# Optimization experiments

Measured on AMD Instinct MI355X. Metric: run time of the kernel, lower is better.

## Reference

```python
import jax, jax.numpy as jnp
import numpy as np

HEADS = 12
LN_EPS = 1e-12
NUM_PROTOTYPES = 8


def _layer_norm(x, g, b):
    mu = x.mean(-1, keepdims=True)
    var = ((x - mu) ** 2).mean(-1, keepdims=True)
    return (x - mu) / jnp.sqrt(var + LN_EPS) * g + b


def _bert_attention(q_in, kv_in, wq, bq, wk, bk, wv, bv, wo, bo, ln_g, ln_b):
    # HF BertAttention: MHA (query from q_in, key/value from kv_in) then
    # SelfOutput: dense + residual(q_in) + LayerNorm. Dropout = 0 (eval).
    B, Sq, D = q_in.shape
    Sk = kv_in.shape[1]
    dh = D // HEADS
    q = (q_in @ wq + bq).reshape(B, Sq, HEADS, dh).transpose(0, 2, 1, 3)
    k = (kv_in @ wk + bk).reshape(B, Sk, HEADS, dh).transpose(0, 2, 1, 3)
    v = (kv_in @ wv + bv).reshape(B, Sk, HEADS, dh).transpose(0, 2, 1, 3)
    scores = jnp.einsum('bhqd,bhkd->bhqk', q, k) / jnp.sqrt(jnp.asarray(dh, q.dtype))
    probs = jax.nn.softmax(scores, axis=-1)
    ctx = jnp.einsum('bhqk,bhkd->bhqd', probs, v).transpose(0, 2, 1, 3).reshape(B, Sq, D)
    return _layer_norm(ctx @ wo + bo + q_in, ln_g, ln_b)


def setup_inputs() -> dict:
    key = jax.random.key(0)
    ks = jax.random.split(key, 16)
    D = 768
    inp = {
        'local_feats': jax.random.normal(ks[0], (8, 256, D), jnp.float32),
        'global_feat_dict': jax.random.normal(ks[1], (16384, D), jnp.float32),
    }
    i = 2
    for pre in ('ll', 'lg'):
        for nm in ('wq', 'wk', 'wv', 'wo'):
            inp[f'{pre}_{nm}'] = 0.02 * jax.random.normal(ks[i], (D, D), jnp.float32)
            i += 1
        for nm in ('bq', 'bk', 'bv', 'bo'):
            inp[f'{pre}_{nm}'] = jnp.zeros((D,), jnp.float32)
        inp[f'{pre}_ln_g'] = jnp.ones((D,), jnp.float32)
        inp[f'{pre}_ln_b'] = jnp.zeros((D,), jnp.float32)
    inp['ln_g'] = jnp.ones((D,), jnp.float32)
    inp['ln_b'] = jnp.zeros((D,), jnp.float32)
    inp['aug_w'] = 0.02 * jax.random.normal(ks[i], (D, 1), jnp.float32)
    inp['ori_w'] = 0.02 * jax.random.normal(ks[i + 1], (D, 1), jnp.float32)
    inp['aug_b'] = jnp.zeros((1,), jnp.float32)
    inp['ori_b'] = jnp.zeros((1,), jnp.float32)
    return inp


def reference(local_feats, global_feat_dict,
              ll_wq, ll_bq, ll_wk, ll_bk, ll_wv, ll_bv, ll_wo, ll_bo, ll_ln_g, ll_ln_b,
              lg_wq, lg_bq, lg_wk, lg_bk, lg_wv, lg_bv, lg_wo, lg_bo, lg_ln_g, lg_ln_b,
              ln_g, ln_b, aug_w, aug_b, ori_w, ori_b):
    B, L, D = local_feats.shape
    K = NUM_PROTOTYPES
    # similarity_topk retrieval: cosine similarity against prototype pool
    g_norm = global_feat_dict / jnp.linalg.norm(global_feat_dict, axis=-1, keepdims=True)
    t_norm = local_feats / jnp.linalg.norm(local_feats, axis=-1, keepdims=True)
    sim = jnp.einsum('bld,nd->bln', t_norm, g_norm)          # [B, L, N]
    topk_idx = jax.lax.top_k(sim, K)[1]                       # [B, L, K]
    global_feats = global_feat_dict[topk_idx].reshape(B, L * K, D)
    # self-attn over locals, cross-attn locals -> retrieved prototypes
    ll = _bert_attention(local_feats, local_feats,
                         ll_wq, ll_bq, ll_wk, ll_bk, ll_wv, ll_bv, ll_wo, ll_bo, ll_ln_g, ll_ln_b)
    lg = _bert_attention(local_feats, global_feats,
                         lg_wq, lg_bq, lg_wk, lg_bk, lg_wv, lg_bv, lg_wo, lg_bo, lg_ln_g, lg_ln_b)
    out = _layer_norm(ll + lg, ln_g, ln_b)
    aug_weight = jax.nn.sigmoid(out @ aug_w + aug_b + local_feats @ ori_w + ori_b)
    return aug_weight * out + (1.0 - aug_weight) * local_feats
```

## Files before the change

### kernel.cpp

```cpp
#include <hip/hip_runtime.h>
#include <math.h>

#define D     768
#define HEADS 12
#define DH    64
#define BATCH 8
#define LSEQ  256
#define MROWS 2048
#define NDICT 16384
#define TOPK  8

typedef _Float16 half_t;
typedef half_t half8 __attribute__((ext_vector_type(8)));
typedef float floatx4 __attribute__((ext_vector_type(4)));

#define F_DICT 0u
#define F_DKV  6291456u
#define F_TN   18874368u
#define F_LOC  19660800u
#define F_WT   20447232u
#define F_BF   22806528u
#define F_TOPI 22814720u
#define F_LP   22831104u
#define F_CTX  25976832u
#define F_D1   26763264u
#define F_D3   28336128u
#define F_ML   31481856u
#define F_CANDV 31678464u
#define F_CANDI 31809536u
#define F_NRM  31940608u
#define F_USED 31956992u
#define F_ROWMAP 31973376u
#define F_INVMAP 31989760u
#define F_CNT  32006144u

typedef const __attribute__((address_space(1))) void* gptr_as1;
typedef __attribute__((address_space(3))) void* lptr_as3;
#define GLDS16(gp, lp) __builtin_amdgcn_global_load_lds((gptr_as1)(gp), (lptr_as3)(lp), 16, 0, 0)

__device__ __forceinline__ float bsum(float v, float* red) {
  int t = threadIdx.x;
#pragma unroll
  for (int d = 32; d > 0; d >>= 1) v += __shfl_xor(v, d);
  if ((t & 63) == 0) red[t >> 6] = v;
  __syncthreads();
  float r = red[0] + red[1] + red[2] + red[3];
  __syncthreads();
  return r;
}

__global__ __launch_bounds__(256) void k_prep_wt(
    const float* __restrict__ dict, const float* __restrict__ local,
    half_t* __restrict__ gdict_h, float* __restrict__ dnrm,
    half_t* __restrict__ loc_h, half_t* __restrict__ tn_h,
    const float* w0, const float* w1, const float* w2, const float* w3,
    const float* w4, const float* w5, const float* w6, const float* w7,
    const float* b0, const float* b1, const float* b2, const float* b3,
    const float* b4, const float* b5, const float* b6, const float* b7,
    half_t* __restrict__ Wt, float* __restrict__ bfout) {
  __shared__ float red[8];
  __shared__ float tile[32][33];
  int g = blockIdx.x, t = threadIdx.x;
  if (g < NDICT) {
    const float* xr = dict + (size_t)g * D;
    float v0 = xr[t], v1 = xr[t + 256], v2 = xr[t + 512];
    float s = bsum(v0*v0 + v1*v1 + v2*v2, red);
    float n = sqrtf(s), inv = 1.0f / n;
    half_t* yr = gdict_h + (size_t)g * D;
    yr[t] = (half_t)(v0*inv); yr[t+256] = (half_t)(v1*inv); yr[t+512] = (half_t)(v2*inv);
    if (t == 0) dnrm[g] = n;
  } else if (g < NDICT + MROWS) {
    size_t r = g - NDICT;
    const float* xr = local + r * (size_t)D;
    float v0 = xr[t], v1 = xr[t + 256], v2 = xr[t + 512];
    float s = bsum(v0*v0 + v1*v1 + v2*v2, red);
    float inv = 1.0f / sqrtf(s);
    half_t* rr = loc_h + r * (size_t)D;
    half_t* nr = tn_h + r * (size_t)D;
    rr[t] = (half_t)v0;        rr[t+256] = (half_t)v1;        rr[t+512] = (half_t)v2;
    nr[t] = (half_t)(v0*inv);  nr[t+256] = (half_t)(v1*inv);  nr[t+512] = (half_t)(v2*inv);
  } else {
    const float* wsrcs[8] = {w0,w1,w2,w3,w4,w5,w6,w7};
    const float* bsrcs[8] = {b0,b1,b2,b3,b4,b5,b6,b7};
    int id = g - (NDICT + MROWS);
    int z = id / 576, rem = id % 576;
    int by = rem / 24, bx = rem % 24;
    const float* Wsrc = wsrcs[z];
    half_t* dst = Wt + (size_t)z * D * D;
    int tx = t & 31, ty = t >> 5;
    int c0 = bx * 32, r0 = by * 32;
#pragma unroll
    for (int j = 0; j < 4; j++)
      tile[ty + j*8][tx] = Wsrc[(size_t)(r0 + ty + j*8) * D + c0 + tx];
    __syncthreads();
#pragma unroll
    for (int j = 0; j < 4; j++)
      dst[(size_t)(c0 + ty + j*8) * D + r0 + tx] = (half_t)tile[tx][ty + j*8];
    if (bx == 0 && by == 0) {
#pragma unroll
      for (int j = 0; j < 3; j++)
        bfout[z * D + t + j*256] = bsrcs[z][t + j*256];
    }
  }
}

__device__ __forceinline__ void hgemm_core(
    const half_t* __restrict__ A, const half_t* __restrict__ B,
    const float* __restrict__ bias, const float* __restrict__ dnrm,
    const int* __restrict__ rowmap, void* __restrict__ Cout,
    int N, int K, int outHalf, int bx, int by, int mhalf,
    half_t* As, half_t* Bs) {
  int tid = threadIdx.x;
  int wid = tid >> 6, lane = tid & 63;
  int l16 = lane & 15, quad = lane >> 4;
  int n0 = bx * 128, m0 = by * 128;
  if (mhalf && m0 >= mhalf) { B += (size_t)D * D; if (bias) bias += D; }
  int wm = (wid & 1) * 64, wn = (wid >> 1) * 64;

  int r0  = tid >> 3;
  int cbg = (tid & 7) ^ (r0 & 7);
  const half_t* Aps[4];
#pragma unroll
  for (int i = 0; i < 4; i++) {
    int mm = m0 + r0 + 32*i;
    int mr = rowmap ? rowmap[mm] : mm;
    Aps[i] = A + (size_t)mr * K + cbg * 8;
  }
  const half_t* Bp = B + (size_t)(n0 + r0) * K + cbg * 8;

  floatx4 acc[4][4];
#pragma unroll
  for (int i = 0; i < 4; i++)
#pragma unroll
    for (int j = 0; j < 4; j++) { acc[i][j][0]=0.f; acc[i][j][1]=0.f; acc[i][j][2]=0.f; acc[i][j][3]=0.f; }

  for (int k0 = 0; k0 < K; k0 += 64) {
#pragma unroll
    for (int i = 0; i < 4; i++)
      GLDS16(Aps[i] + k0, As + ((size_t)i*256 + wid*64) * 8);
#pragma unroll
    for (int i = 0; i < 4; i++)
      GLDS16(Bp + k0 + (size_t)i * 32 * K, Bs + ((size_t)i*256 + wid*64) * 8);
    __syncthreads();
#pragma unroll
    for (int ks = 0; ks < 2; ks++) {
      half8 af[4], bf[4];
#pragma unroll
      for (int i = 0; i < 4; i++) {
        int row = wm + i*16 + l16;
        int cb = (quad + ks*4) ^ (row & 7);
        af[i] = *(const half8*)&As[row*64 + cb*8];
      }
#pragma unroll
      for (int j = 0; j < 4; j++) {
        int row = wn + j*16 + l16;
        int cb = (quad + ks*4) ^ (row & 7);
        bf[j] = *(const half8*)&Bs[row*64 + cb*8];
      }
#pragma unroll
      for (int i = 0; i < 4; i++)
#pragma unroll
        for (int j = 0; j < 4; j++)
          acc[i][j] = __builtin_amdgcn_mfma_f32_16x16x32_f16(af[i], bf[j], acc[i][j], 0, 0, 0);
    }
    __syncthreads();
  }

  float bcol[4];
#pragma unroll
  for (int j = 0; j < 4; j++) bcol[j] = bias ? bias[n0 + wn + j*16 + l16] : 0.f;
  if (outHalf) {
    half_t* C = (half_t*)Cout;
#pragma unroll
    for (int i = 0; i < 4; i++)
#pragma unroll
      for (int r = 0; r < 4; r++) {
        int grow = m0 + wm + i*16 + quad*4 + r;
        float sc = dnrm ? dnrm[rowmap ? rowmap[grow] : grow] : 1.0f;
#pragma unroll
        for (int j = 0; j < 4; j++)
          C[(size_t)grow * N + n0 + wn + j*16 + l16] = (half_t)(acc[i][j][r] * sc + bcol[j]);
      }
  } else {
    float* C = (float*)Cout;
#pragma unroll
    for (int i = 0; i < 4; i++)
#pragma unroll
      for (int r = 0; r < 4; r++) {
        int grow = m0 + wm + i*16 + quad*4 + r;
        float sc = dnrm ? dnrm[rowmap ? rowmap[grow] : grow] : 1.0f;
#pragma unroll
        for (int j = 0; j < 4; j++)
          C[(size_t)grow * N + n0 + wn + j*16 + l16] = acc[i][j][r] * sc + bcol[j];
      }
  }
}

__global__ __launch_bounds__(256) void k_gemm_simlp(
    const half_t* __restrict__ tn, const half_t* __restrict__ gd,
    half_t* __restrict__ sim,
    const half_t* __restrict__ loc, const half_t* __restrict__ wt0,
    const float* __restrict__ bf0, half_t* __restrict__ lp) {
  __shared__ half_t As[128*64];
  __shared__ half_t Bs[128*64];
  int gid = blockIdx.x;
  if (gid < 2048) {
    int bx = (gid & 7) + ((gid >> 3) / 16) * 8;
    int by = (gid >> 3) % 16;
    hgemm_core(tn, gd, nullptr, nullptr, nullptr, sim, NDICT, D, 1, bx, by, 0, As, Bs);
  } else {
    int rel = gid - 2048;
    int bx = (rel & 7) + ((rel >> 3) / 16) * 8;
    int by = (rel >> 3) % 16;
    hgemm_core(loc, wt0, bf0, nullptr, nullptr, lp, 3072, D, 1, bx, by, 0, As, Bs);
  }
}

__global__ __launch_bounds__(256) void k_gemm_dkv(
    const half_t* __restrict__ gd, const half_t* __restrict__ wt4,
    const float* __restrict__ bf4, const float* __restrict__ dnrm,
    const int* __restrict__ rowmap, const int* __restrict__ cnt,
    half_t* __restrict__ dkv) {
  __shared__ half_t As[128*64];
  __shared__ half_t Bs[128*64];
  int mceil = (*cnt + 127) & ~127;
  if ((int)blockIdx.y * 128 >= mceil) return;
  hgemm_core(gd, wt4, bf4, dnrm, rowmap, dkv, 1536, D, 1, blockIdx.x, blockIdx.y, 0, As, Bs);
}

__global__ __launch_bounds__(256) void k_gemm_wo(
    const half_t* __restrict__ ctx, const half_t* __restrict__ wt6,
    const float* __restrict__ bf6, float* __restrict__ dd) {
  __shared__ half_t As[128*64];
  __shared__ half_t Bs[128*64];
  hgemm_core(ctx, wt6, bf6, nullptr, nullptr, dd, D, D, 0, blockIdx.x, blockIdx.y, MROWS, As, Bs);
}

__global__ __launch_bounds__(256) void k_topk1(const half_t* __restrict__ sim,
                                               float* __restrict__ candv,
                                               int* __restrict__ candi,
                                               int* __restrict__ used,
                                               int* __restrict__ rowmap,
                                               int* __restrict__ cnt) {
  int t = threadIdx.x;
  if (t < 4) used[blockIdx.x * 4 + t] = 0;
  else if (t < 8) rowmap[blockIdx.x * 4 + t - 4] = 0;
  if (blockIdx.x == 0 && t == 8) *cnt = 0;

  int gw = blockIdx.x * 4 + (t >> 6);
  int lane = t & 63;
  int row = gw >> 3, seg = gw & 7;
  int cbase = seg * 2048;
  const half_t* p = sim + (size_t)row * NDICT + cbase;

  float v[32];
#pragma unroll
  for (int i = 0; i < 4; i++) {
    half8 h = *(const half8*)(p + i*512 + lane*8);
#pragma unroll
    for (int j = 0; j < 8; j++) v[i*8 + j] = (float)h[j];
  }
  float m = v[0]; int pos = 0;
#pragma unroll
  for (int i = 1; i < 32; i++) { if (v[i] > m) { m = v[i]; pos = i; } }

  for (int it = 0; it < 8; it++) {
    int gidx = cbase + (pos >> 3) * 512 + lane * 8 + (pos & 7);
    float bv = m; int bi = gidx;
#pragma unroll
    for (int d2 = 1; d2 < 64; d2 <<= 1) {
      float ov = __shfl_xor(bv, d2); int oi = __shfl_xor(bi, d2);
      if (ov > bv || (ov == bv && oi < bi)) { bv = ov; bi = oi; }
    }
    if (lane == 0) {
      size_t base = (size_t)row * 64 + seg * 8 + it;
      candv[base] = bv; candi[base] = bi;
    }
    if (bi == gidx) {
      v[pos] = -INFINITY;
      m = v[0]; pos = 0;
#pragma unroll
      for (int i = 1; i < 32; i++) { if (v[i] > m) { m = v[i]; pos = i; } }
    }
  }
}

__global__ __launch_bounds__(256) void k_topk2(const float* __restrict__ candv,
                                               const int* __restrict__ candi,
                                               int* __restrict__ topi,
                                               int* __restrict__ used) {
  int row = blockIdx.x * 4 + (threadIdx.x >> 6);
  int lane = threadIdx.x & 63;
  float v = candv[(size_t)row * 64 + lane];
  int id = candi[(size_t)row * 64 + lane];
#pragma unroll
  for (int it = 0; it < 8; it++) {
    float bv = v; int bi = id;
#pragma unroll
    for (int d2 = 1; d2 < 64; d2 <<= 1) {
      float ov = __shfl_xor(bv, d2); int oi = __shfl_xor(bi, d2);
      if (ov > bv || (ov == bv && oi < bi)) { bv = ov; bi = oi; }
    }
    if (lane == 0) { topi[row * 8 + it] = bi; used[bi] = 1; }
    if (id == bi) { v = -INFINITY; id = 0x7FFFFFFF; }
  }
}

__global__ __launch_bounds__(256) void k_cmp(const int* __restrict__ used,
                                             int* __restrict__ rowmap,
                                             int* __restrict__ invmap,
                                             int* __restrict__ cnt) {
  int i = blockIdx.x * 256 + threadIdx.x;
  if (used[i]) { int s = atomicAdd(cnt, 1); rowmap[s] = i; invmap[i] = s; }
}
__global__ __launch_bounds__(256) void k_remap(int* __restrict__ topi,
                                               const int* __restrict__ invmap) {
  int i = blockIdx.x * 256 + threadIdx.x;
  topi[i] = invmap[topi[i]];
}

__global__ __launch_bounds__(256) void k_flash2(
    const half_t* __restrict__ lp, const half_t* __restrict__ dkv,
    const int* __restrict__ topi_,
    half_t* __restrict__ ctx_ll, half_t* __restrict__ Opart, float* __restrict__ ml) {
  __shared__ half_t Ks[64][72];
  __shared__ half_t Vt[64][72];
  __shared__ half_t Ps[4][16][72];

  int tid = threadIdx.x;
  int wid = tid >> 6;
  int lane = tid & 63;
  int l16 = lane & 15, quad = lane >> 4;

  const half_t *Q, *K, *V; const int* kidx; half_t* Out;
  int qS, kvS, Sk, ns, rel;
  if (blockIdx.x < BATCH*HEADS*4*4) {
    rel = blockIdx.x;
    Q = lp + 2304; qS = 3072; K = dkv; V = dkv + 768; kvS = 1536;
    kidx = topi_; Sk = LSEQ*TOPK; ns = 4; Out = nullptr;
  } else {
    rel = blockIdx.x - BATCH*HEADS*4*4;
    Q = lp; qS = 3072; K = lp + 768; V = lp + 1536; kvS = 3072;
    kidx = nullptr; Sk = LSEQ; ns = 1; Out = ctx_ll;
  }

  int sp = rel % ns;
  int rest = rel / ns;
  int qt = rest & 3;
  int h  = (rest >> 2) % HEADS;
  int bb = rest / (4 * HEADS);
  int q0 = qt * 64 + wid * 16;
  int sLen = Sk / ns, s0 = sp * sLen;

  const float SCL = 0.125f * 1.4426950408889634f;
  const half_t* qrow = Q + (size_t)(bb * LSEQ + q0 + l16) * qS + h * DH;
  half8 aq0 = *(const half8*)(qrow + quad*8);
  half8 aq1 = *(const half8*)(qrow + 32 + quad*8);

  floatx4 o[4];
#pragma unroll
  for (int nt = 0; nt < 4; nt++) { o[nt][0]=0.f; o[nt][1]=0.f; o[nt][2]=0.f; o[nt][3]=0.f; }
  float mreg[4] = {-INFINITY, -INFINITY, -INFINITY, -INFINITY};
  float lreg[4] = {0.f, 0.f, 0.f, 0.f};

  for (int k0 = s0; k0 < s0 + sLen; k0 += 64) {
    {
      int row = tid >> 2, cg = tid & 3;
      int key = k0 + row;
      size_t rowid = kidx ? (size_t)kidx[(size_t)bb * Sk + key]
                          : (size_t)(bb * LSEQ + key);
      const half_t* kb = K + rowid * (size_t)kvS + h * DH + cg * 16;
      const half_t* vb = V + rowid * (size_t)kvS + h * DH + cg * 16;
      *(half8*)&Ks[row][cg*16]     = *(const half8*)kb;
      *(half8*)&Ks[row][cg*16 + 8] = *(const half8*)(kb + 8);
      half8 v0 = *(const half8*)vb, v1 = *(const half8*)(vb + 8);
#pragma unroll
      for (int jj = 0; jj < 8; jj++) { Vt[cg*16 + jj][row] = v0[jj]; Vt[cg*16 + 8 + jj][row] = v1[jj]; }
    }
    __syncthreads();

    floatx4 c[4];
#pragma unroll
    for (int nt = 0; nt < 4; nt++) {
      half8 b0 = *(const half8*)&Ks[nt*16 + l16][quad*8];
      half8 b1 = *(const half8*)&Ks[nt*16 + l16][32 + quad*8];
      floatx4 z; z[0]=0.f; z[1]=0.f; z[2]=0.f; z[3]=0.f;
      z = __builtin_amdgcn_mfma_f32_16x16x32_f16(aq0, b0, z, 0, 0, 0);
      z = __builtin_amdgcn_mfma_f32_16x16x32_f16(aq1, b1, z, 0, 0, 0);
      c[nt] = z;
    }

    float alpha[4];
#pragma unroll
    for (int r = 0; r < 4; r++) {
      float mx = fmaxf(fmaxf(c[0][r], c[1][r]), fmaxf(c[2][r], c[3][r]));
      mx = fmaxf(mx, __shfl_xor(mx, 1));
      mx = fmaxf(mx, __shfl_xor(mx, 2));
      mx = fmaxf(mx, __shfl_xor(mx, 4));
      mx = fmaxf(mx, __shfl_xor(mx, 8));
      float mn = fmaxf(mreg[r], mx);
      float al = __builtin_amdgcn_exp2f((mreg[r] - mn) * SCL);
      float ps = 0.f;
#pragma unroll
      for (int nt = 0; nt < 4; nt++) {
        float p = __builtin_amdgcn_exp2f((c[nt][r] - mn) * SCL);
        c[nt][r] = p; ps += p;
      }
      ps += __shfl_xor(ps, 1);
      ps += __shfl_xor(ps, 2);
      ps += __shfl_xor(ps, 4);
      ps += __shfl_xor(ps, 8);
      mreg[r] = mn; lreg[r] = lreg[r] * al + ps; alpha[r] = al;
    }

#pragma unroll
    for (int nt = 0; nt < 4; nt++)
#pragma unroll
      for (int r = 0; r < 4; r++)
        Ps[wid][quad*4 + r][nt*16 + l16] = (half_t)c[nt][r];
    half8 p0 = *(const half8*)&Ps[wid][l16][quad*8];
    half8 p1 = *(const half8*)&Ps[wid][l16][32 + quad*8];

#pragma unroll
    for (int nt = 0; nt < 4; nt++)
#pragma unroll
      for (int r = 0; r < 4; r++) o[nt][r] *= alpha[r];
#pragma unroll
    for (int nt = 0; nt < 4; nt++) {
      half8 v0 = *(const half8*)&Vt[nt*16 + l16][quad*8];
      half8 v1 = *(const half8*)&Vt[nt*16 + l16][32 + quad*8];
      o[nt] = __builtin_amdgcn_mfma_f32_16x16x32_f16(p0, v0, o[nt], 0, 0, 0);
      o[nt] = __builtin_amdgcn_mfma_f32_16x16x32_f16(p1, v1, o[nt], 0, 0, 0);
    }
    __syncthreads();
  }

  if (ns == 1) {
    half_t* ob = Out + (size_t)(bb * LSEQ + q0 + quad*4) * D + h * DH;
#pragma unroll
    for (int r = 0; r < 4; r++) {
      float inv = 1.0f / lreg[r];
#pragma unroll
      for (int nt = 0; nt < 4; nt++)
        ob[(size_t)r * D + nt*16 + l16] = (half_t)(o[nt][r] * inv);
    }
  } else {
    size_t rbase = (size_t)sp * MROWS + bb * LSEQ + q0 + quad*4;
    half_t* ob = Opart + rbase * D + h * DH;
#pragma unroll
    for (int r = 0; r < 4; r++) {
      float inv = 1.0f / lreg[r];
#pragma unroll
      for (int nt = 0; nt < 4; nt++)
        ob[(size_t)r * D + nt*16 + l16] = (half_t)(o[nt][r] * inv);
    }
    if (l16 == 0) {
#pragma unroll
      for (int r = 0; r < 4; r++) {
        size_t mi = ((rbase + r) * HEADS + h) * 2;
        ml[mi] = mreg[r]; ml[mi + 1] = lreg[r];
      }
    }
  }
}

__global__ __launch_bounds__(256) void k_comb(const half_t* __restrict__ Op,
                                              const float* __restrict__ ml,
                                              half_t* __restrict__ ctx) {
  int r = blockIdx.x, t = threadIdx.x;
  const float SCL = 0.125f * 1.4426950408889634f;
#pragma unroll
  for (int i = 0; i < 3; i++) {
    int col = t + i*256;
    int h = col >> 6;
    float m[4], l[4];
    float ms = -INFINITY;
#pragma unroll
    for (int s = 0; s < 4; s++) {
      size_t mi = (((size_t)s * MROWS + r) * HEADS + h) * 2;
      m[s] = ml[mi]; l[s] = ml[mi + 1];
      ms = fmaxf(ms, m[s]);
    }
    float den = 0.f, num = 0.f;
#pragma unroll
    for (int s = 0; s < 4; s++) {
      float w = __builtin_amdgcn_exp2f((m[s] - ms) * SCL) * l[s];
      den += w;
      num += w * (float)Op[((size_t)s * MROWS + r) * D + col];
    }
    ctx[(size_t)r * D + col] = (half_t)(num / den);
  }
}

__global__ __launch_bounds__(256) void k_lngate3(
    const float* __restrict__ dd, const float* __restrict__ loc,
    const float* __restrict__ llg, const float* __restrict__ llb,
    const float* __restrict__ lgg, const float* __restrict__ lgb,
    const float* __restrict__ lng, const float* __restrict__ lnb,
    const float* __restrict__ aw, const float* __restrict__ ow,
    const float* __restrict__ ab, const float* __restrict__ orb,
    float* __restrict__ y) {
  __shared__ float red[8];
  size_t r = blockIdx.x; int t = threadIdx.x;
  const float* ar = dd + r*(size_t)D;
  const float* br = dd + ((size_t)MROWS + r)*(size_t)D;
  const float* lcl = loc + r*(size_t)D;
  float l0 = lcl[t], l1 = lcl[t+256], l2 = lcl[t+512];

  float a0 = ar[t]+l0, a1 = ar[t+256]+l1, a2 = ar[t+512]+l2;
  float mu = bsum(a0+a1+a2, red) * (1.0f/768.0f);
  float d0 = a0-mu, d1 = a1-mu, d2 = a2-mu;
  float var = bsum(d0*d0 + d1*d1 + d2*d2, red) * (1.0f/768.0f);
  float rstd = rsqrtf(var + 1e-12f);
  float x0 = d0*rstd*llg[t]     + llb[t];
  float x1 = d1*rstd*llg[t+256] + llb[t+256];
  float x2 = d2*rstd*llg[t+512] + llb[t+512];

  float b0 = br[t]+l0, b1 = br[t+256]+l1, b2 = br[t+512]+l2;
  mu = bsum(b0+b1+b2, red) * (1.0f/768.0f);
  d0 = b0-mu; d1 = b1-mu; d2 = b2-mu;
  var = bsum(d0*d0 + d1*d1 + d2*d2, red) * (1.0f/768.0f);
  rstd = rsqrtf(var + 1e-12f);
  x0 += d0*rstd*lgg[t]     + lgb[t];
  x1 += d1*rstd*lgg[t+256] + lgb[t+256];
  x2 += d2*rstd*lgg[t+512] + lgb[t+512];

  mu = bsum(x0+x1+x2, red) * (1.0f/768.0f);
  d0 = x0-mu; d1 = x1-mu; d2 = x2-mu;
  var = bsum(d0*d0 + d1*d1 + d2*d2, red) * (1.0f/768.0f);
  rstd = rsqrtf(var + 1e-12f);
  float o0 = d0*rstd*lng[t]     + lnb[t];
  float o1 = d1*rstd*lng[t+256] + lnb[t+256];
  float o2 = d2*rstd*lng[t+512] + lnb[t+512];

  float s = o0*aw[t] + l0*ow[t]
          + o1*aw[t+256] + l1*ow[t+256]
          + o2*aw[t+512] + l2*ow[t+512];
  float z = bsum(s, red) + ab[0] + orb[0];
  float w = 1.0f / (1.0f + __expf(-z));
  float* yr = y + r*(size_t)D;
  yr[t]     = w*o0 + (1.f-w)*l0;
  yr[t+256] = w*o1 + (1.f-w)*l1;
  yr[t+512] = w*o2 + (1.f-w)*l2;
}

extern "C" void kernel_launch(void* const* d_in, const int* in_sizes, int n_in,
                              void* d_out, int out_size, void* d_ws, size_t ws_size,
                              hipStream_t stream) {
  (void)in_sizes; (void)n_in; (void)out_size; (void)ws_size;
  const float* local = (const float*)d_in[0];
  const float* dict  = (const float*)d_in[1];
  const float* ll_g  = (const float*)d_in[10];
  const float* ll_b  = (const float*)d_in[11];
  const float* lg_g  = (const float*)d_in[20];
  const float* lg_b  = (const float*)d_in[21];
  const float* ln_g  = (const float*)d_in[22];
  const float* ln_b  = (const float*)d_in[23];
  const float* aug_w = (const float*)d_in[24];
  const float* ori_w = (const float*)d_in[25];
  const float* aug_b = (const float*)d_in[26];
  const float* ori_b = (const float*)d_in[27];

  float* W = (float*)d_ws;
  half_t* gdict_h = (half_t*)(W + F_DICT);
  half_t* sim_h   = (half_t*)(W + F_DKV);
  half_t* dkv     = (half_t*)(W + F_DKV);
  half_t* tn_h    = (half_t*)(W + F_TN);
  half_t* loc_h   = (half_t*)(W + F_LOC);
  half_t* wt      = (half_t*)(W + F_WT);
  float*  bf      = W + F_BF;
  int*    topi    = (int*)(W + F_TOPI);
  half_t* lp      = (half_t*)(W + F_LP);
  half_t* ctx_ll  = (half_t*)(W + F_CTX);
  half_t* ctx_lg  = (half_t*)(W + F_D1);
  half_t* Opart   = (half_t*)(W + F_D1);
  float*  dd      = W + F_D3;
  float*  ml      = W + F_ML;
  float*  candv   = W + F_CANDV;
  int*    candi   = (int*)(W + F_CANDI);
  float*  dnrm    = W + F_NRM;
  int*    used    = (int*)(W + F_USED);
  int*    rowmap  = (int*)(W + F_ROWMAP);
  int*    invmap  = (int*)(W + F_INVMAP);
  int*    cnt     = (int*)(W + F_CNT);

  dim3 blk(256);
  const size_t WS = (size_t)D * D;

  k_prep_wt<<<NDICT + MROWS + 4608, blk, 0, stream>>>(
      dict, local, gdict_h, dnrm, loc_h, tn_h,
      (const float*)d_in[2], (const float*)d_in[3], (const float*)d_in[4],
      (const float*)d_in[12], (const float*)d_in[13], (const float*)d_in[14],
      (const float*)d_in[5], (const float*)d_in[15],
      (const float*)d_in[6], (const float*)d_in[7], (const float*)d_in[8],
      (const float*)d_in[16], (const float*)d_in[17], (const float*)d_in[18],
      (const float*)d_in[9], (const float*)d_in[19], wt, bf);

  k_gemm_simlp<<<2048 + 384, blk, 0, stream>>>(tn_h, gdict_h, sim_h,
                                               loc_h, wt + 0*WS, bf + 0, lp);

  k_topk1<<<MROWS*8/4, blk, 0, stream>>>(sim_h, candv, candi, used, rowmap, cnt);
  k_topk2<<<MROWS/4, blk, 0, stream>>>(candv, candi, topi, used);
  k_cmp<<<64, blk, 0, stream>>>(used, rowmap, invmap, cnt);
  k_remap<<<64, blk, 0, stream>>>(topi, invmap);

  k_gemm_dkv<<<dim3(12, 128), blk, 0, stream>>>(
      gdict_h, wt + 4*WS, bf + 3072, dnrm, rowmap, cnt, dkv);

  k_flash2<<<dim3(BATCH*HEADS*4*4 + BATCH*HEADS*4), blk, 0, stream>>>(
      lp, dkv, topi, ctx_ll, Opart, ml);
  k_comb<<<MROWS, blk, 0, stream>>>(Opart, ml, ctx_lg);

  k_gemm_wo<<<dim3(6, 32), blk, 0, stream>>>(ctx_ll, wt + 6*WS, bf + 4608, dd);

  k_lngate3<<<MROWS, blk, 0, stream>>>(dd, local,
      ll_g, ll_b, lg_g, lg_b, ln_g, ln_b,
      aug_w, ori_w, aug_b, ori_b, (float*)d_out);
}
```

Before: 434.6 us.

## Use 256x256 double-buffered 512-thread GEMM tiles for similarity and KV projections

Adds a new GEMM core that computes 256x256 output tiles with 512 threads and double-buffered LDS staging via direct global-to-LDS loads, so the next K-slice loads while MFMAs run. The similarity/local-projection GEMM and the dictionary KV GEMM now use it, with a new XCD-aware block swizzle and fewer, larger blocks. The workspace is relaid out so the sim, dkv and dd buffers alias. Larger tiles cut global traffic per FLOP but use much more LDS and registers per block, which lowers occupancy. The candidate-skip granularity in the dkv GEMM also becomes coarser (256 rows).

```diff
diff --git a/kernel.cpp b/kernel.cpp
--- a/kernel.cpp
+++ b/kernel.cpp
@@ -14,25 +14,24 @@
 typedef half_t half8 __attribute__((ext_vector_type(8)));
 typedef float floatx4 __attribute__((ext_vector_type(4)));
 
-#define F_DICT 0u
-#define F_DKV  6291456u
-#define F_TN   18874368u
-#define F_LOC  19660800u
-#define F_WT   20447232u
-#define F_BF   22806528u
-#define F_TOPI 22814720u
-#define F_LP   22831104u
-#define F_CTX  25976832u
-#define F_D1   26763264u
-#define F_D3   28336128u
-#define F_ML   31481856u
-#define F_CANDV 31678464u
-#define F_CANDI 31809536u
-#define F_NRM  31940608u
-#define F_USED 31956992u
-#define F_ROWMAP 31973376u
-#define F_INVMAP 31989760u
-#define F_CNT  32006144u
+#define F_DICT   0u
+#define F_TN     6291456u
+#define F_LOC    7077888u
+#define F_WT     7864320u
+#define F_BF     10223616u
+#define F_TOPI   10231808u
+#define F_LP     10248192u
+#define F_SIM    13393920u
+#define F_CTX    30171136u
+#define F_D1     30957568u
+#define F_CANDV  30957568u
+#define F_CANDI  31088640u
+#define F_ML     34103296u
+#define F_NRM    34299904u
+#define F_USED   34316288u
+#define F_ROWMAP 34332672u
+#define F_INVMAP 34349056u
+#define F_CNT    34365440u
 
 typedef const __attribute__((address_space(1))) void* gptr_as1;
 typedef __attribute__((address_space(3))) void* lptr_as3;
@@ -196,36 +195,146 @@
   }
 }
 
-__global__ __launch_bounds__(256) void k_gemm_simlp(
+__device__ __forceinline__ void hgemm256_core(
+    const half_t* __restrict__ A, const half_t* __restrict__ B,
+    const float* __restrict__ bias, const float* __restrict__ dnrm,
+    const int* __restrict__ rowmap, half_t* __restrict__ C,
+    int N, int K, int bx, int by,
+    half_t* As0, half_t* As1, half_t* Bs0, half_t* Bs1) {
+  const int tid = threadIdx.x;
+  const int wid = tid >> 6, lane = tid & 63;
+  const int l16 = lane & 15, quad = lane >> 4;
+  const int m0 = by * 256, n0 = bx * 256;
+
+  const int r0 = tid >> 3;
+  const int cg = (tid & 7) ^ (r0 & 7);
+  const half_t* Aps[4]; const half_t* Bps[4];
+#pragma unroll
+  for (int i = 0; i < 4; i++) {
+    int mm = m0 + r0 + i * 64;
+    int mr = rowmap ? rowmap[mm] : mm;
+    Aps[i] = A + (size_t)mr * K + cg * 8;
+    Bps[i] = B + (size_t)(n0 + r0 + i * 64) * K + cg * 8;
+  }
+
+  const int arow = (wid & 3) * 32 + l16;
+  const int brow = (wid >> 2) * 64 + l16;
+  const int cb0 = (quad ^ (l16 & 7)) * 8;
+  const int cb1 = ((quad + 4) ^ (l16 & 7)) * 8;
+
+  floatx4 acc[4][2][4];
+#pragma unroll
+  for (int q = 0; q < 4; q++)
+#pragma unroll
+    for (int mi = 0; mi < 2; mi++)
+#pragma unroll
+      for (int ni = 0; ni < 4; ni++) {
+        acc[q][mi][ni][0] = 0.f; acc[q][mi][ni][1] = 0.f;
+        acc[q][mi][ni][2] = 0.f; acc[q][mi][ni][3] = 0.f;
+      }
+  half8 af[2][2], bf[4][2];
+
+#define STAGE(Adst, Bdst, kn) { \
+    GLDS16(Aps[0] + (kn), (Adst) + (0*512 + wid*64) * 8); \
+    GLDS16(Aps[1] + (kn), (Adst) + (1*512 + wid*64) * 8); \
+    GLDS16(Aps[2] + (kn), (Adst) + (2*512 + wid*64) * 8); \
+    GLDS16(Aps[3] + (kn), (Adst) + (3*512 + wid*64) * 8); \
+    GLDS16(Bps[0] + (kn), (Bdst) + (0*512 + wid*64) * 8); \
+    GLDS16(Bps[1] + (kn), (Bdst) + (1*512 + wid*64) * 8); \
+    GLDS16(Bps[2] + (kn), (Bdst) + (2*512 + wid*64) * 8); \
+    GLDS16(Bps[3] + (kn), (Bdst) + (3*512 + wid*64) * 8); }
+#define LDA(qm) { const int rb_ = (qm)*8192 + arow*64; \
+    af[0][0] = *(const half8*)&Ar[rb_ + cb0];        af[0][1] = *(const half8*)&Ar[rb_ + cb1]; \
+    af[1][0] = *(const half8*)&Ar[rb_ + 1024 + cb0]; af[1][1] = *(const half8*)&Ar[rb_ + 1024 + cb1]; }
+#define LDB(qn) { const int rb_ = (qn)*8192 + brow*64; \
+    bf[0][0] = *(const half8*)&Br[rb_ + cb0];        bf[0][1] = *(const half8*)&Br[rb_ + cb1]; \
+    bf[1][0] = *(const half8*)&Br[rb_ + 1024 + cb0]; bf[1][1] = *(const half8*)&Br[rb_ + 1024 + cb1]; \
+    bf[2][0] = *(const half8*)&Br[rb_ + 2048 + cb0]; bf[2][1] = *(const half8*)&Br[rb_ + 2048 + cb1]; \
+    bf[3][0] = *(const half8*)&Br[rb_ + 3072 + cb0]; bf[3][1] = *(const half8*)&Br[rb_ + 3072 + cb1]; }
+#define MM(q) { _Pragma("unroll") for (int mi = 0; mi < 2; mi++) { \
+    _Pragma("unroll") for (int ni = 0; ni < 4; ni++) { \
+      acc[q][mi][ni] = __builtin_amdgcn_mfma_f32_16x16x32_f16(af[mi][0], bf[ni][0], acc[q][mi][ni], 0, 0, 0); \
+      acc[q][mi][ni] = __builtin_amdgcn_mfma_f32_16x16x32_f16(af[mi][1], bf[ni][1], acc[q][mi][ni], 0, 0, 0); } } }
+
+  const int NT = K >> 6;
+  STAGE(As0, Bs0, 0);
+  __syncthreads();
+
+  half_t* Ar = As0; half_t* Aw = As1;
+  half_t* Br = Bs0; half_t* Bw = Bs1;
+  for (int t = 0; t < NT; ++t) {
+    if (t + 1 < NT) STAGE(Aw, Bw, (t + 1) * 64);
+    LDA(0); LDB(0); MM(0);
+    LDB(1);         MM(1);
+    LDA(1);         MM(2);
+    LDB(0);         MM(3);
+    if (t + 1 < NT) __syncthreads();
+    half_t* tp = Ar; Ar = Aw; Aw = tp;
+    tp = Br; Br = Bw; Bw = tp;
+  }
+
+  float bcol[2][4];
+#pragma unroll
+  for (int qn = 0; qn < 2; qn++)
+#pragma unroll
+    for (int ni = 0; ni < 4; ni++)
+      bcol[qn][ni] = bias ? bias[n0 + qn*128 + (wid >> 2)*64 + ni*16 + l16] : 0.f;
+#pragma unroll
+  for (int q = 0; q < 4; q++) {
+    const int qm = q >> 1;
+    const int qn = (q == 1 || q == 2) ? 1 : 0;
+#pragma unroll
+    for (int mi = 0; mi < 2; mi++)
+#pragma unroll
+      for (int r = 0; r < 4; r++) {
+        int grow = m0 + qm*128 + (wid & 3)*32 + mi*16 + quad*4 + r;
+        float sc = dnrm ? dnrm[rowmap ? rowmap[grow] : grow] : 1.0f;
+#pragma unroll
+        for (int ni = 0; ni < 4; ni++)
+          C[(size_t)grow * N + n0 + qn*128 + (wid >> 2)*64 + ni*16 + l16] =
+              (half_t)(acc[q][mi][ni][r] * sc + bcol[qn][ni]);
+      }
+  }
+#undef STAGE
+#undef LDA
+#undef LDB
+#undef MM
+}
+
+__global__ __launch_bounds__(512) void k_gemm_simlp(
     const half_t* __restrict__ tn, const half_t* __restrict__ gd,
     half_t* __restrict__ sim,
     const half_t* __restrict__ loc, const half_t* __restrict__ wt0,
     const float* __restrict__ bf0, half_t* __restrict__ lp) {
-  __shared__ half_t As[128*64];
-  __shared__ half_t Bs[128*64];
+  __shared__ half_t As[2][256*64];
+  __shared__ half_t Bs[2][256*64];
   int gid = blockIdx.x;
-  if (gid < 2048) {
-    int bx = (gid & 7) + ((gid >> 3) / 16) * 8;
-    int by = (gid >> 3) % 16;
-    hgemm_core(tn, gd, nullptr, nullptr, nullptr, sim, NDICT, D, 1, bx, by, 0, As, Bs);
+  int swz = (gid & 7) * 76 + (gid >> 3);
+  if (swz < 512) {
+    int bx = (swz & 7) + ((swz >> 3) >> 3) * 8;
+    int by = (swz >> 3) & 7;
+    hgemm256_core(tn, gd, nullptr, nullptr, nullptr, sim, NDICT, D, bx, by,
+                  As[0], As[1], Bs[0], Bs[1]);
   } else {
-    int rel = gid - 2048;
-    int bx = (rel & 7) + ((rel >> 3) / 16) * 8;
-    int by = (rel >> 3) % 16;
-    hgemm_core(loc, wt0, bf0, nullptr, nullptr, lp, 3072, D, 1, bx, by, 0, As, Bs);
-  }
-}
-
-__global__ __launch_bounds__(256) void k_gemm_dkv(
+    int rel = swz - 512;
+    int bx = rel >> 3;
+    int by = rel & 7;
+    hgemm256_core(loc, wt0, bf0, nullptr, nullptr, lp, 3072, D, bx, by,
+                  As[0], As[1], Bs[0], Bs[1]);
+  }
+}
+
+__global__ __launch_bounds__(512) void k_gemm_dkv(
     const half_t* __restrict__ gd, const half_t* __restrict__ wt4,
     const float* __restrict__ bf4, const float* __restrict__ dnrm,
     const int* __restrict__ rowmap, const int* __restrict__ cnt,
     half_t* __restrict__ dkv) {
-  __shared__ half_t As[128*64];
-  __shared__ half_t Bs[128*64];
-  int mceil = (*cnt + 127) & ~127;
-  if ((int)blockIdx.y * 128 >= mceil) return;
-  hgemm_core(gd, wt4, bf4, dnrm, rowmap, dkv, 1536, D, 1, blockIdx.x, blockIdx.y, 0, As, Bs);
+  __shared__ half_t As[2][256*64];
+  __shared__ half_t Bs[2][256*64];
+  int mceil = (*cnt + 255) & ~255;
+  if ((int)blockIdx.y * 256 >= mceil) return;
+  hgemm256_core(gd, wt4, bf4, dnrm, rowmap, dkv, 1536, D,
+                blockIdx.x, blockIdx.y, As[0], As[1], Bs[0], Bs[1]);
 }
 
 __global__ __launch_bounds__(256) void k_gemm_wo(
@@ -563,21 +672,21 @@
 
   float* W = (float*)d_ws;
   half_t* gdict_h = (half_t*)(W + F_DICT);
-  half_t* sim_h   = (half_t*)(W + F_DKV);
-  half_t* dkv     = (half_t*)(W + F_DKV);
   half_t* tn_h    = (half_t*)(W + F_TN);
   half_t* loc_h   = (half_t*)(W + F_LOC);
   half_t* wt      = (half_t*)(W + F_WT);
   float*  bf      = W + F_BF;
   int*    topi    = (int*)(W + F_TOPI);
   half_t* lp      = (half_t*)(W + F_LP);
+  half_t* sim_h   = (half_t*)(W + F_SIM);
+  half_t* dkv     = (half_t*)(W + F_SIM);
+  float*  dd      = W + F_SIM;
   half_t* ctx_ll  = (half_t*)(W + F_CTX);
   half_t* ctx_lg  = (half_t*)(W + F_D1);
   half_t* Opart   = (half_t*)(W + F_D1);
-  float*  dd      = W + F_D3;
-  float*  ml      = W + F_ML;
   float*  candv   = W + F_CANDV;
   int*    candi   = (int*)(W + F_CANDI);
+  float*  ml      = W + F_ML;
   float*  dnrm    = W + F_NRM;
   int*    used    = (int*)(W + F_USED);
   int*    rowmap  = (int*)(W + F_ROWMAP);
@@ -585,6 +694,7 @@
   int*    cnt     = (int*)(W + F_CNT);
 
   dim3 blk(256);
+  dim3 blk5(512);
   const size_t WS = (size_t)D * D;
 
   k_prep_wt<<<NDICT + MROWS + 4608, blk, 0, stream>>>(
@@ -596,15 +706,15 @@
       (const float*)d_in[16], (const float*)d_in[17], (const float*)d_in[18],
       (const float*)d_in[9], (const float*)d_in[19], wt, bf);
 
-  k_gemm_simlp<<<2048 + 384, blk, 0, stream>>>(tn_h, gdict_h, sim_h,
-                                               loc_h, wt + 0*WS, bf + 0, lp);
+  k_gemm_simlp<<<512 + 96, blk5, 0, stream>>>(tn_h, gdict_h, sim_h,
+                                              loc_h, wt + 0*WS, bf + 0, lp);
 
   k_topk1<<<MROWS*8/4, blk, 0, stream>>>(sim_h, candv, candi, used, rowmap, cnt);
   k_topk2<<<MROWS/4, blk, 0, stream>>>(candv, candi, topi, used);
   k_cmp<<<64, blk, 0, stream>>>(used, rowmap, invmap, cnt);
   k_remap<<<64, blk, 0, stream>>>(topi, invmap);
 
-  k_gemm_dkv<<<dim3(12, 128), blk, 0, stream>>>(
+  k_gemm_dkv<<<dim3(6, 64), blk5, 0, stream>>>(
       gdict_h, wt + 4*WS, bf + 3072, dnrm, rowmap, cnt, dkv);
 
   k_flash2<<<dim3(BATCH*HEADS*4*4 + BATCH*HEADS*4), blk, 0, stream>>>(
```

Measured after the change: 428.5 us. About the same (-1.4%).
